# Kernel optimization log

Hardware: AMD Instinct MI355X
Metric: run time of the kernel (lower is better)

The kernel has to match this reference:

```python
import jax, jax.numpy as jnp
import numpy as np

# static sizes
B, N_PER, D, H, L, DFF, IN_DIM = 32, 1024, 128, 4, 3, 2048, 64
N = B * N_PER
HD = D // H
EPS = 1e-5


def setup_inputs() -> dict:
    key = jax.random.key(0)
    ks = jax.random.split(key, 16)
    s = 0.02
    rn = lambda k, shp: jax.random.normal(k, shp, jnp.float32) * s
    return {
        "x": jax.random.normal(ks[0], (N, IN_DIM), jnp.float32),
        # uniform graph sizes -> static max_nodes; sorted graph ids
        "batch": jnp.repeat(jnp.arange(B, dtype=jnp.int32), N_PER),
        "W_in": rn(ks[1], (D, IN_DIM)),
        "b_in": rn(ks[2], (D,)),
        "Wqkv": rn(ks[3], (L, 3 * D, D)),
        "bqkv": rn(ks[4], (L, 3 * D)),
        "Wo": rn(ks[5], (L, D, D)),
        "bo": rn(ks[6], (L, D)),
        "W1": rn(ks[7], (L, DFF, D)),
        "b1": rn(ks[8], (L, DFF)),
        "W2": rn(ks[9], (L, D, DFF)),
        "b2": rn(ks[10], (L, D)),
        "ln1_g": jnp.ones((L, D), jnp.float32),
        "ln1_b": jnp.zeros((L, D), jnp.float32),
        "ln2_g": jnp.ones((L, D), jnp.float32),
        "ln2_b": jnp.zeros((L, D), jnp.float32),
    }


def _ln(x, g, b):
    m = x.mean(-1, keepdims=True)
    v = jnp.mean((x - m) ** 2, axis=-1, keepdims=True)
    return (x - m) / jnp.sqrt(v + EPS) * g + b


def _mha(h, Wqkv, bqkv, Wo, bo):
    # h: [B, S, D]
    qkv = h @ Wqkv.T + bqkv                      # [B, S, 3D]
    q, k, v = jnp.split(qkv, 3, axis=-1)
    q = q.reshape(B, -1, H, HD)
    k = k.reshape(B, -1, H, HD)
    v = v.reshape(B, -1, H, HD)
    att = jnp.einsum("bqhd,bkhd->bhqk", q, k) / np.sqrt(HD).astype(np.float32)
    p = jax.nn.softmax(att, axis=-1)
    o = jnp.einsum("bhqk,bkhd->bqhd", p, v).reshape(B, -1, D)
    return o @ Wo.T + bo


def reference(x, batch, W_in, b_in, Wqkv, bqkv, Wo, bo, W1, b1, W2, b2,
              ln1_g, ln1_b, ln2_g, ln2_b):
    # fused ragged -> padded: project all nodes once, scatter by (graph, pos)
    h = x @ W_in.T + b_in                        # [N, D]
    starts = jnp.searchsorted(batch, jnp.arange(B, dtype=batch.dtype))
    pos = jnp.arange(N, dtype=batch.dtype) - starts[batch]
    padded = jnp.zeros((B, N_PER, D), h.dtype).at[batch, pos].set(h)

    out = padded
    for l in range(L):  # post-LN TransformerEncoderLayer, dropout=eval
        a = _mha(out, Wqkv[l], bqkv[l], Wo[l], bo[l])
        out = _ln(out + a, ln1_g[l], ln1_b[l])
        f = jax.nn.relu(out @ W1[l].T + b1[l]) @ W2[l].T + b2[l]
        out = _ln(out + f, ln2_g[l], ln2_b[l])

    # mask derived from projected inputs, exactly as the original
    mask = (padded.sum(axis=2) != 0).astype(out.dtype)  # [B, S]
    return (out * mask[:, :, None]).sum(axis=1) / mask.sum(axis=1, keepdims=True)
```

## Files before the change

### kernel.cpp

```cpp
#include <hip/hip_runtime.h>
#include <hip/hip_bf16.h>
#include <stdint.h>

#define BB    32
#define NPER  1024
#define NTOT  32768
#define DD    128
#define HH    4
#define HD    32
#define LL    3
#define DFF   2048
#define INDIM 64
#define QKSCALE 0.17677669529663687f

typedef unsigned short u16;
typedef short bf16x8 __attribute__((ext_vector_type(8)));
typedef float f32x4 __attribute__((ext_vector_type(4)));

#define AS_GLOBAL(p) ((const __attribute__((address_space(1))) void*)(p))
#define AS_LDS(p)    ((__attribute__((address_space(3))) void*)(p))

__device__ __forceinline__ float bf2f(u16 v){
  unsigned u = ((unsigned)v) << 16; float f; __builtin_memcpy(&f, &u, 4); return f;
}
__device__ __forceinline__ u16 f2bf(float f){
  unsigned u; __builtin_memcpy(&u, &f, 4);
  unsigned lsb = (u >> 16) & 1u;
  u += 0x7fffu + lsb;
  return (u16)(u >> 16);
}

constexpr size_t OFF_FLAG   = 0;
constexpr size_t OFF_STARTS = 256;
constexpr size_t OFF_BIN    = 1024;
constexpr size_t OFF_BQKV   = OFF_BIN   + 128*4;
constexpr size_t OFF_BO     = OFF_BQKV  + 1152*4;
constexpr size_t OFF_B1     = OFF_BO    + 384*4;
constexpr size_t OFF_B2     = OFF_B1    + 6144*4;
constexpr size_t OFF_LN1G   = OFF_B2    + 384*4;
constexpr size_t OFF_LN1B   = OFF_LN1G  + 384*4;
constexpr size_t OFF_LN2G   = OFF_LN1B  + 384*4;
constexpr size_t OFF_LN2B   = OFF_LN2G  + 384*4;
constexpr size_t OFF_XB     = 40960;
constexpr size_t OFF_WINB   = OFF_XB    + (size_t)2097152*2;
constexpr size_t OFF_WQKVB  = OFF_WINB  + (size_t)8192*2;
constexpr size_t OFF_WOB    = OFF_WQKVB + (size_t)147456*2;
constexpr size_t OFF_W1B    = OFF_WOB   + (size_t)49152*2;
constexpr size_t OFF_W2B    = OFF_W1B   + (size_t)786432*2;
constexpr size_t OFF_CUR    = OFF_W2B   + (size_t)786432*2;
constexpr size_t OFF_TMP    = OFF_CUR   + (size_t)4194304*4;
constexpr size_t OFF_CURB   = OFF_TMP   + (size_t)4194304*4;
constexpr size_t OFF_QKVB   = OFF_CURB  + (size_t)4194304*2;
constexpr size_t OFF_ATTNOB = OFF_QKVB  + (size_t)12582912*2;
constexpr size_t OFF_ACTB   = OFF_ATTNOB+ (size_t)4194304*2;
constexpr size_t OFF_MASK   = OFF_ACTB  + (size_t)16777216*2;
constexpr size_t OFF_VT     = OFF_MASK  + (size_t)NTOT*4;
constexpr size_t OFF_RED    = OFF_VT    + (size_t)4096*1024*2;
constexpr size_t OFF_CNT    = OFF_RED   + (size_t)32*8*128*4;

__device__ __forceinline__ int plaus(unsigned bits){
  if ((bits << 1) == 0u) return 1;
  unsigned e = (bits >> 23) & 0xFFu;
  return (e >= 100u && e <= 140u) ? 1 : 0;
}
__global__ void prep_kernel(const unsigned* __restrict__ x, const int* __restrict__ batch,
                            int* __restrict__ flag, int* __restrict__ starts){
  __shared__ int red[256];
  int t = threadIdx.x, c = 0;
  for (int i = t; i < 2048; i += 256){
    unsigned w = x[i];
    c += (plaus(w << 16) & plaus(w & 0xFFFF0000u));
  }
  red[t] = c; __syncthreads();
  for (int s = 128; s > 0; s >>= 1){ if (t < s) red[t] += red[t+s]; __syncthreads(); }
  if (t == 0) *flag = (red[0] >= 1229) ? 1 : 0;
  if (t < BB){
    int lo = 0, hi = NTOT;
    while (lo < hi){ int mid = (lo + hi) >> 1; if (batch[mid] < t) lo = mid + 1; else hi = mid; }
    starts[t] = lo;
  }
}

struct ConvSeg { const void* src; void* dst; int n; int tobf; };
struct ConvArgs { ConvSeg s[14]; };

__global__ __launch_bounds__(256) void convall_kernel(ConvArgs a, const int* __restrict__ flag){
  const int isb = *flag;
  const int blk = blockIdx.x;
  int seg = -1, base = 0, lb = 0;
  #pragma unroll
  for (int i = 0; i < 14; ++i){
    int nb = (a.s[i].n + 1023) >> 10;
    if (seg < 0){
      if (blk < base + nb){ seg = i; lb = blk - base; }
      base += nb;
    }
  }
  const ConvSeg sg = a.s[seg];
  const int idx = lb*1024 + threadIdx.x*4;
  if (idx >= sg.n) return;
  if (sg.tobf){
    u16* dst = (u16*)sg.dst + idx;
    if (isb){
      *(uint2*)dst = *(const uint2*)((const u16*)sg.src + idx);
    } else {
      const float* s4 = (const float*)sg.src + idx;
      dst[0] = f2bf(s4[0]); dst[1] = f2bf(s4[1]);
      dst[2] = f2bf(s4[2]); dst[3] = f2bf(s4[3]);
    }
  } else {
    float* dst = (float*)sg.dst + idx;
    if (isb){
      const u16* s4 = (const u16*)sg.src + idx;
      dst[0] = bf2f(s4[0]); dst[1] = bf2f(s4[1]);
      dst[2] = bf2f(s4[2]); dst[3] = bf2f(s4[3]);
    } else {
      *(float4*)dst = *(const float4*)((const float*)sg.src + idx);
    }
  }
}

__global__ __launch_bounds__(256) void inproj_kernel(
    const void* __restrict__ xraw,
    const u16* __restrict__ WINB,
    const float* __restrict__ bin,
    const int* __restrict__ batch, const int* __restrict__ starts,
    const int* __restrict__ flag,
    float* __restrict__ cur, u16* __restrict__ curb, float* __restrict__ mask)
{
  __shared__ __align__(16) u16 Wl[8192];
  const int t = threadIdx.x, wave = t >> 6, lane = t & 63;
  const int quad = lane >> 4, l16 = lane & 15;
  const int m0 = blockIdx.x * 64;
  const int isb = *flag;

  #pragma unroll
  for (int j = 0; j < 4; ++j){
    int s = t + 256*j;
    int r = s >> 3, c8 = (s & 7) ^ (r & 7);
    *(uint4*)&Wl[s*8] = *(const uint4*)(WINB + (size_t)r*INDIM + c8*8);
  }
  bf16x8 af[2];
  const int arow = m0 + wave*16 + l16;
  if (isb){
    const u16* XB = (const u16*)xraw;
    #pragma unroll
    for (int kk = 0; kk < 2; ++kk)
      af[kk] = *(const bf16x8*)(XB + (size_t)arow*INDIM + kk*32 + quad*8);
  } else {
    const float* Xf = (const float*)xraw;
    #pragma unroll
    for (int kk = 0; kk < 2; ++kk){
      float4 a = *(const float4*)(Xf + (size_t)arow*INDIM + kk*32 + quad*8);
      float4 b = *(const float4*)(Xf + (size_t)arow*INDIM + kk*32 + quad*8 + 4);
      af[kk][0] = (short)f2bf(a.x); af[kk][1] = (short)f2bf(a.y);
      af[kk][2] = (short)f2bf(a.z); af[kk][3] = (short)f2bf(a.w);
      af[kk][4] = (short)f2bf(b.x); af[kk][5] = (short)f2bf(b.y);
      af[kk][6] = (short)f2bf(b.z); af[kk][7] = (short)f2bf(b.w);
    }
  }
  __syncthreads();

  f32x4 O[8];
  #pragma unroll
  for (int nt = 0; nt < 8; ++nt){ O[nt][0]=0.f; O[nt][1]=0.f; O[nt][2]=0.f; O[nt][3]=0.f; }

  #pragma unroll
  for (int nt = 0; nt < 8; ++nt){
    int row = nt*16 + l16;
    bf16x8 wf[2];
    #pragma unroll
    for (int kk = 0; kk < 2; ++kk)
      wf[kk] = *(const bf16x8*)&Wl[(row*8 + ((kk*4 + quad) ^ (row & 7)))*8];
    #pragma unroll
    for (int kk = 0; kk < 2; ++kk)
      O[nt] = __builtin_amdgcn_mfma_f32_16x16x32_bf16(af[kk], wf[kk], O[nt], 0, 0, 0);
  }

  #pragma unroll
  for (int rr = 0; rr < 4; ++rr){
    int node = m0 + wave*16 + quad*4 + rr;
    int gr = batch[node];
    int p  = node - starts[gr];
    float vs[8], sum = 0.f;
    #pragma unroll
    for (int nt = 0; nt < 8; ++nt){
      float v = O[nt][rr] + bin[nt*16 + l16];
      vs[nt] = v; sum += v;
    }
    sum += __shfl_xor(sum, 1); sum += __shfl_xor(sum, 2);
    sum += __shfl_xor(sum, 4); sum += __shfl_xor(sum, 8);
    if ((unsigned)p < (unsigned)NPER && (unsigned)gr < (unsigned)BB){
      size_t j = (size_t)gr*NPER + p;
      #pragma unroll
      for (int nt = 0; nt < 8; ++nt){
        int col = nt*16 + l16;
        cur[j*DD + col]  = vs[nt];
        curb[j*DD + col] = f2bf(vs[nt]);
      }
      if (l16 == 0) mask[j] = (sum != 0.f) ? 1.f : 0.f;
    }
  }
}

__global__ __launch_bounds__(256) void fattn_kernel(
    const u16* __restrict__ qkvb,
    const u16* __restrict__ vt,
    u16* __restrict__ attnob)
{
  __shared__ __align__(16) u16 Klds[2][2048];
  __shared__ __align__(16) u16 Vl[2][2048];
  __shared__ __align__(16) u16 Pl[4][2][16*72];

  const int t = threadIdx.x;
  const int wave = t >> 6, lane = t & 63;
  const int quad = lane >> 4, l16 = lane & 15;
  const int q0 = blockIdx.x * 128;
  const int h = blockIdx.y, b = blockIdx.z;
  const size_t qkvbase = (size_t)b * NPER * 384;
  const u16* Kg = qkvb + qkvbase + 128 + h*HD;
  const u16* Vg = vt + (size_t)((b*HH + h)*HD) * NPER;

  bf16x8 qf[2];
  #pragma unroll
  for (int qt = 0; qt < 2; ++qt){
    const u16* qp = qkvb + qkvbase + (size_t)(q0 + wave*32 + qt*16 + l16)*384 + h*HD + quad*8;
    uint4 qv = *(const uint4*)qp;
    u16 raw[8]; __builtin_memcpy(raw, &qv, 16);
    #pragma unroll
    for (int j = 0; j < 8; ++j) qf[qt][j] = (short)f2bf(bf2f(raw[j]) * QKSCALE);
  }

  const int vcv = wave*2 + (lane >> 5), vd = lane & 31;
  auto stage = [&](int buf, int kt){
    __builtin_amdgcn_global_load_lds(
        AS_GLOBAL(Kg + (size_t)(kt*64 + lane)*384 + wave*8),
        AS_LDS(&Klds[buf][wave*64*8]), 16, 0, 0);
    __builtin_amdgcn_global_load_lds(
        AS_GLOBAL(Vg + (size_t)vd*NPER + kt*64 + vcv*8),
        AS_LDS(&Vl[buf][wave*64*8]), 16, 0, 0);
  };

  float lsum[2] = {0.f, 0.f};
  f32x4 o[2][2];
  #pragma unroll
  for (int qt = 0; qt < 2; ++qt)
    #pragma unroll
    for (int i = 0; i < 2; ++i){ o[qt][i][0]=0.f; o[qt][i][1]=0.f; o[qt][i][2]=0.f; o[qt][i][3]=0.f; }

  stage(0, 0);
  asm volatile("s_waitcnt vmcnt(0)" ::: "memory");
  __syncthreads();

  for (int kt = 0; kt < 16; ++kt){
    const int buf = kt & 1;
    if (kt + 1 < 16) stage(buf ^ 1, kt + 1);

    f32x4 sfr[2][4];
    #pragma unroll
    for (int nt = 0; nt < 4; ++nt){
      bf16x8 kf = *(const bf16x8*)&Klds[buf][(quad*64 + nt*16 + l16)*8];
      f32x4 z = {0.f,0.f,0.f,0.f};
      sfr[0][nt] = __builtin_amdgcn_mfma_f32_16x16x32_bf16(kf, qf[0], z, 0, 0, 0);
      sfr[1][nt] = __builtin_amdgcn_mfma_f32_16x16x32_bf16(kf, qf[1], z, 0, 0, 0);
    }

    #pragma unroll
    for (int qt = 0; qt < 2; ++qt){
      float ps = 0.f;
      #pragma unroll
      for (int nt = 0; nt < 4; ++nt){
        float e0 = __expf(sfr[qt][nt][0]), e1 = __expf(sfr[qt][nt][1]);
        float e2 = __expf(sfr[qt][nt][2]), e3 = __expf(sfr[qt][nt][3]);
        ps += (e0 + e1) + (e2 + e3);
        uint2 w;
        w.x = (unsigned)f2bf(e0) | ((unsigned)f2bf(e1) << 16);
        w.y = (unsigned)f2bf(e2) | ((unsigned)f2bf(e3) << 16);
        *(uint2*)&Pl[wave][qt][l16*72 + nt*16 + quad*4] = w;
      }
      ps += __shfl_xor(ps, 16);
      ps += __shfl_xor(ps, 32);
      lsum[qt] += ps;
    }
    asm volatile("s_waitcnt lgkmcnt(0)" ::: "memory");

    #pragma unroll
    for (int kk = 0; kk < 2; ++kk){
      bf16x8 v0 = *(const bf16x8*)&Vl[buf][((kk*4 + quad)*32 + l16)*8];
      bf16x8 v1 = *(const bf16x8*)&Vl[buf][((kk*4 + quad)*32 + 16 + l16)*8];
      #pragma unroll
      for (int qt = 0; qt < 2; ++qt){
        bf16x8 pf = *(const bf16x8*)&Pl[wave][qt][l16*72 + kk*32 + quad*8];
        o[qt][0] = __builtin_amdgcn_mfma_f32_16x16x32_bf16(pf, v0, o[qt][0], 0, 0, 0);
        o[qt][1] = __builtin_amdgcn_mfma_f32_16x16x32_bf16(pf, v1, o[qt][1], 0, 0, 0);
      }
    }

    if (kt + 1 < 16){
      asm volatile("s_waitcnt vmcnt(0)" ::: "memory");
      __syncthreads();
    }
  }

  #pragma unroll
  for (int qt = 0; qt < 2; ++qt){
    #pragma unroll
    for (int r = 0; r < 4; ++r){
      float inv = 1.f / __shfl(lsum[qt], quad*4 + r);
      int row = q0 + wave*32 + qt*16 + quad*4 + r;
      size_t base = (size_t)(b*NPER + row)*DD + h*HD;
      attnob[base + l16]      = f2bf(o[qt][0][r] * inv);
      attnob[base + 16 + l16] = f2bf(o[qt][1][r] * inv);
    }
  }
}

__global__ __launch_bounds__(256) void wgemm2_kernel(
    const u16* __restrict__ A,
    const u16* __restrict__ Wbase,
    const float* __restrict__ biasb,
    u16* __restrict__ outb, int opitch,
    u16* __restrict__ vtout)
{
  __shared__ __align__(16) u16 Wl[16384];
  const int t = threadIdx.x, wave = t >> 6, lane = t & 63;
  const int quad = lane >> 4, l16 = lane & 15;
  const int m0 = blockIdx.x * 128, nb = blockIdx.y;
  const u16* Wsl = Wbase + (size_t)nb * 16384;
  const float* bias = biasb + nb * 128;

  #pragma unroll
  for (int j = 0; j < 8; ++j){
    int s = t + 256*j;
    int r = s >> 4, cx = (s & 15) ^ (r & 15);
    *(uint4*)&Wl[s*8] = *(const uint4*)(Wsl + (size_t)r*128 + cx*8);
  }
  bf16x8 af[2][4];
  #pragma unroll
  for (int mt = 0; mt < 2; ++mt)
    #pragma unroll
    for (int kk = 0; kk < 4; ++kk)
      af[mt][kk] = *(const bf16x8*)(A + (size_t)(m0 + wave*32 + mt*16 + l16)*128 + kk*32 + quad*8);
  __syncthreads();

  f32x4 O[2][8];
  #pragma unroll
  for (int mt = 0; mt < 2; ++mt)
    #pragma unroll
    for (int nt = 0; nt < 8; ++nt){ O[mt][nt][0]=0.f; O[mt][nt][1]=0.f; O[mt][nt][2]=0.f; O[mt][nt][3]=0.f; }

  #pragma unroll
  for (int nt = 0; nt < 8; ++nt){
    int row = nt*16 + l16;
    bf16x8 wf[4];
    #pragma unroll
    for (int kk = 0; kk < 4; ++kk)
      wf[kk] = *(const bf16x8*)&Wl[(row*16 + ((kk*4 + quad) ^ l16))*8];
    #pragma unroll
    for (int mt = 0; mt < 2; ++mt)
      #pragma unroll
      for (int kk = 0; kk < 4; ++kk)
        O[mt][nt] = __builtin_amdgcn_mfma_f32_16x16x32_bf16(af[mt][kk], wf[kk], O[mt][nt], 0, 0, 0);
  }

  if (nb == 2){
    #pragma unroll
    for (int mt = 0; mt < 2; ++mt){
      int rowb = m0 + wave*32 + mt*16 + quad*4;
      int bg = rowb >> 10, s = rowb & 1023;
      #pragma unroll
      for (int nt = 0; nt < 8; ++nt){
        int col = nt*16 + l16;
        int hh = col >> 5, d = col & 31;
        float v0 = O[mt][nt][0] + bias[col], v1 = O[mt][nt][1] + bias[col];
        float v2 = O[mt][nt][2] + bias[col], v3 = O[mt][nt][3] + bias[col];
        uint2 w;
        w.x = (unsigned)f2bf(v0) | ((unsigned)f2bf(v1) << 16);
        w.y = (unsigned)f2bf(v2) | ((unsigned)f2bf(v3) << 16);
        *(uint2*)(vtout + (size_t)((bg*HH + hh)*HD + d)*NPER + s) = w;
      }
    }
  } else {
    #pragma unroll
    for (int mt = 0; mt < 2; ++mt)
      #pragma unroll
      for (int rr = 0; rr < 4; ++rr){
        int row = m0 + wave*32 + mt*16 + quad*4 + rr;
        #pragma unroll
        for (int nt = 0; nt < 8; ++nt){
          int col = nt*16 + l16;
          outb[(size_t)row*opitch + nb*128 + col] = f2bf(O[mt][nt][rr] + bias[col]);
        }
      }
  }
}

__global__ __launch_bounds__(256, 2) void ffn_kernel(
    const u16* __restrict__ attnob,
    const u16* __restrict__ Wog,
    const float* __restrict__ bo,
    const float* __restrict__ g1, const float* __restrict__ beta1,
    const u16* __restrict__ W1g,
    const u16* __restrict__ W2g,
    const float* __restrict__ b1,
    const float* __restrict__ b2,
    const float* __restrict__ g2, const float* __restrict__ beta2,
    float* __restrict__ cur, u16* __restrict__ curb)
{
  __shared__ __align__(16) u16 SM[37376];
  const int t = threadIdx.x, wave = t >> 6, lane = t & 63;
  const int quad = lane >> 4, l16 = lane & 15;
  const int m0 = blockIdx.x * 64;
  u16* Pw = &SM[32768 + wave*1152];

  #pragma unroll
  for (int i = 0; i < 8; ++i){
    int s0 = wave*512 + i*64;
    int s = s0 + lane;
    int r = s >> 4, cx = (s & 15) ^ (r & 15);
    __builtin_amdgcn_global_load_lds(
        AS_GLOBAL(Wog + (size_t)r*128 + cx*8),
        AS_LDS(&SM[16384 + s0*8]), 16, 0, 0);
  }
  bf16x8 afo[4];
  #pragma unroll
  for (int kk = 0; kk < 4; ++kk)
    afo[kk] = *(const bf16x8*)(attnob + (size_t)(m0 + wave*16 + l16)*128 + kk*32 + quad*8);
  asm volatile("s_waitcnt vmcnt(0)" ::: "memory");
  __syncthreads();

  f32x4 O[8];
  #pragma unroll
  for (int nt = 0; nt < 8; ++nt){ O[nt][0]=0.f; O[nt][1]=0.f; O[nt][2]=0.f; O[nt][3]=0.f; }
  #pragma unroll
  for (int nt = 0; nt < 8; ++nt){
    int row = nt*16 + l16;
    bf16x8 wf[4];
    #pragma unroll
    for (int kk = 0; kk < 4; ++kk)
      wf[kk] = *(const bf16x8*)&SM[16384 + (row*16 + ((kk*4 + quad) ^ l16))*8];
    #pragma unroll
    for (int kk = 0; kk < 4; ++kk)
      O[nt] = __builtin_amdgcn_mfma_f32_16x16x32_bf16(afo[kk], wf[kk], O[nt], 0, 0, 0);
  }

  float res[8][4];
  u16* Tw = &SM[wave*2176];
  #pragma unroll
  for (int rr = 0; rr < 4; ++rr){
    int row = m0 + wave*16 + quad*4 + rr;
    float vs[8], sum = 0.f;
    #pragma unroll
    for (int nt = 0; nt < 8; ++nt){
      int col = nt*16 + l16;
      float v = O[nt][rr] + bo[col] + cur[(size_t)row*DD + col];
      vs[nt] = v; sum += v;
    }
    sum += __shfl_xor(sum, 1); sum += __shfl_xor(sum, 2);
    sum += __shfl_xor(sum, 4); sum += __shfl_xor(sum, 8);
    float mean = sum * (1.f/DD);
    float sq = 0.f;
    #pragma unroll
    for (int nt = 0; nt < 8; ++nt){ float d = vs[nt] - mean; sq += d*d; }
    sq += __shfl_xor(sq, 1); sq += __shfl_xor(sq, 2);
    sq += __shfl_xor(sq, 4); sq += __shfl_xor(sq, 8);
    float rs = rsqrtf(sq * (1.f/DD) + 1e-5f);
    #pragma unroll
    for (int nt = 0; nt < 8; ++nt){
      int col = nt*16 + l16;
      float o = (vs[nt] - mean)*rs*g1[col] + beta1[col];
      res[nt][rr] = o;
      Tw[(quad*4 + rr)*136 + col] = f2bf(o);
    }
  }
  asm volatile("s_waitcnt lgkmcnt(0)" ::: "memory");

  bf16x8 af[4];
  #pragma unroll
  for (int kk = 0; kk < 4; ++kk)
    af[kk] = *(const bf16x8*)&Tw[l16*136 + kk*32 + quad*8];
  __syncthreads();

  auto stage = [&](int buf, int dffc){
    #pragma unroll
    for (int i = 0; i < 4; ++i){
      const int s0 = wave*256 + i*64;
      const int s  = s0 + lane;
      { int r = s >> 4, cx = (s & 15) ^ (r & 15);
        __builtin_amdgcn_global_load_lds(
            AS_GLOBAL(W1g + (size_t)(dffc + r)*128 + cx*8),
            AS_LDS(&SM[buf*8192 + s0*8]), 16, 0, 0); }
      { int r = s >> 3, cx = (s & 7) ^ (r & 7);
        __builtin_amdgcn_global_load_lds(
            AS_GLOBAL(W2g + (size_t)r*DFF + dffc + cx*8),
            AS_LDS(&SM[16384 + buf*8192 + s0*8]), 16, 0, 0); }
    }
  };

  #pragma unroll
  for (int nt = 0; nt < 8; ++nt){ O[nt][0]=0.f; O[nt][1]=0.f; O[nt][2]=0.f; O[nt][3]=0.f; }

  stage(0, 0);
  asm volatile("s_waitcnt vmcnt(0)" ::: "memory");
  __syncthreads();

  for (int c = 0; c < 32; ++c){
    const int buf = c & 1;
    if (c + 1 < 32) stage(buf ^ 1, (c + 1)*64);

    #pragma unroll
    for (int nt = 0; nt < 4; ++nt){
      int row = nt*16 + l16;
      bf16x8 wf[4];
      #pragma unroll
      for (int kk = 0; kk < 4; ++kk)
        wf[kk] = *(const bf16x8*)&SM[buf*8192 + (row*16 + ((kk*4 + quad) ^ l16))*8];
      float b1v = b1[c*64 + row];
      f32x4 s = {0.f,0.f,0.f,0.f};
      #pragma unroll
      for (int kk = 0; kk < 4; ++kk)
        s = __builtin_amdgcn_mfma_f32_16x16x32_bf16(af[kk], wf[kk], s, 0, 0, 0);
      #pragma unroll
      for (int rr = 0; rr < 4; ++rr)
        Pw[(quad*4 + rr)*72 + nt*16 + l16] = f2bf(fmaxf(s[rr] + b1v, 0.f));
    }
    asm volatile("s_waitcnt lgkmcnt(0)" ::: "memory");

    bf16x8 pf[2];
    #pragma unroll
    for (int kk = 0; kk < 2; ++kk)
      pf[kk] = *(const bf16x8*)&Pw[l16*72 + kk*32 + quad*8];
    #pragma unroll
    for (int nt = 0; nt < 8; ++nt){
      int row = nt*16 + l16;
      bf16x8 wf[2];
      #pragma unroll
      for (int kk = 0; kk < 2; ++kk)
        wf[kk] = *(const bf16x8*)&SM[16384 + buf*8192 + (row*8 + ((kk*4 + quad) ^ (l16 & 7)))*8];
      #pragma unroll
      for (int kk = 0; kk < 2; ++kk)
        O[nt] = __builtin_amdgcn_mfma_f32_16x16x32_bf16(pf[kk], wf[kk], O[nt], 0, 0, 0);
    }

    if (c + 1 < 32){
      asm volatile("s_waitcnt vmcnt(0)" ::: "memory");
      __syncthreads();
    }
  }

  #pragma unroll
  for (int rr = 0; rr < 4; ++rr){
    int row = m0 + wave*16 + quad*4 + rr;
    float vs[8], sum = 0.f;
    #pragma unroll
    for (int nt = 0; nt < 8; ++nt){
      int col = nt*16 + l16;
      float v = O[nt][rr] + b2[col] + res[nt][rr];
      vs[nt] = v; sum += v;
    }
    sum += __shfl_xor(sum, 1); sum += __shfl_xor(sum, 2);
    sum += __shfl_xor(sum, 4); sum += __shfl_xor(sum, 8);
    float mean = sum * (1.f/DD);
    float sq = 0.f;
    #pragma unroll
    for (int nt = 0; nt < 8; ++nt){ float d = vs[nt] - mean; sq += d*d; }
    sq += __shfl_xor(sq, 1); sq += __shfl_xor(sq, 2);
    sq += __shfl_xor(sq, 4); sq += __shfl_xor(sq, 8);
    float rs = rsqrtf(sq * (1.f/DD) + 1e-5f);
    #pragma unroll
    for (int nt = 0; nt < 8; ++nt){
      int col = nt*16 + l16;
      float o = (vs[nt] - mean)*rs*g2[col] + beta2[col];
      cur[(size_t)row*DD + col]  = o;
      curb[(size_t)row*DD + col] = f2bf(o);
    }
  }
}

__global__ __launch_bounds__(128) void reduce1_kernel(
    const float* __restrict__ cur, const float* __restrict__ mask,
    float* __restrict__ partial, float* __restrict__ cnt)
{
  int b = blockIdx.x, c = blockIdx.y, t = threadIdx.x;
  float acc = 0.f, cn = 0.f;
  for (int s = c*128; s < c*128 + 128; ++s){
    float mk = mask[b*NPER + s];
    acc += cur[(size_t)(b*NPER + s)*DD + t] * mk;
    cn += mk;
  }
  partial[(size_t)(b*8 + c)*DD + t] = acc;
  if (t == 0) cnt[b*8 + c] = cn;
}
__global__ __launch_bounds__(128) void reduce2_kernel(
    const float* __restrict__ partial, const float* __restrict__ cnt,
    const int* __restrict__ flag, void* __restrict__ out)
{
  int b = blockIdx.x, t = threadIdx.x;
  float acc = 0.f, cn = 0.f;
  #pragma unroll
  for (int c = 0; c < 8; ++c){
    acc += partial[(size_t)(b*8 + c)*DD + t];
    cn  += cnt[b*8 + c];
  }
  float val = acc / cn;
  if (*flag) ((u16*)out)[b*DD + t] = f2bf(val);
  else       ((float*)out)[b*DD + t] = val;
}

extern "C" void kernel_launch(void* const* d_in, const int* in_sizes, int n_in,
                              void* d_out, int out_size, void* d_ws, size_t ws_size,
                              hipStream_t stream)
{
  (void)in_sizes; (void)n_in; (void)out_size; (void)ws_size;
  char* ws = (char*)d_ws;
  int*   flag   = (int*)(ws + OFF_FLAG);
  int*   starts = (int*)(ws + OFF_STARTS);
  float* BIN  = (float*)(ws + OFF_BIN);
  float* BQKV = (float*)(ws + OFF_BQKV);
  float* BO   = (float*)(ws + OFF_BO);
  float* B1   = (float*)(ws + OFF_B1);
  float* B2   = (float*)(ws + OFF_B2);
  float* LN1G = (float*)(ws + OFF_LN1G);
  float* LN1B = (float*)(ws + OFF_LN1B);
  float* LN2G = (float*)(ws + OFF_LN2G);
  float* LN2B = (float*)(ws + OFF_LN2B);
  u16* WINB  = (u16*)(ws + OFF_WINB);
  u16* WQKVB = (u16*)(ws + OFF_WQKVB);
  u16* WOB   = (u16*)(ws + OFF_WOB);
  u16* W1B   = (u16*)(ws + OFF_W1B);
  u16* W2B   = (u16*)(ws + OFF_W2B);
  float* CUR = (float*)(ws + OFF_CUR);
  u16* CURB  = (u16*)(ws + OFF_CURB);
  u16* QKVB  = (u16*)(ws + OFF_QKVB);
  u16* ATTNOB= (u16*)(ws + OFF_ATTNOB);
  float* MASK= (float*)(ws + OFF_MASK);
  u16* VT    = (u16*)(ws + OFF_VT);
  float* RED = (float*)(ws + OFF_RED);
  float* CNT = (float*)(ws + OFF_CNT);

  prep_kernel<<<1, 256, 0, stream>>>((const unsigned*)d_in[0], (const int*)d_in[1],
                                     flag, starts);

  ConvArgs ca;
  ca.s[0]  = { d_in[2],  WINB,  DD*INDIM,   1 };
  ca.s[1]  = { d_in[4],  WQKVB, LL*3*DD*DD, 1 };
  ca.s[2]  = { d_in[6],  WOB,   LL*DD*DD,   1 };
  ca.s[3]  = { d_in[8],  W1B,   LL*DFF*DD,  1 };
  ca.s[4]  = { d_in[10], W2B,   LL*DD*DFF,  1 };
  ca.s[5]  = { d_in[3],  BIN,   DD,         0 };
  ca.s[6]  = { d_in[5],  BQKV,  LL*3*DD,    0 };
  ca.s[7]  = { d_in[7],  BO,    LL*DD,      0 };
  ca.s[8]  = { d_in[9],  B1,    LL*DFF,     0 };
  ca.s[9]  = { d_in[11], B2,    LL*DD,      0 };
  ca.s[10] = { d_in[12], LN1G,  LL*DD,      0 };
  ca.s[11] = { d_in[13], LN1B,  LL*DD,      0 };
  ca.s[12] = { d_in[14], LN2G,  LL*DD,      0 };
  ca.s[13] = { d_in[15], LN2B,  LL*DD,      0 };
  int nblk = 0;
  for (int i = 0; i < 14; ++i) nblk += (ca.s[i].n + 1023) >> 10;
  convall_kernel<<<nblk, 256, 0, stream>>>(ca, flag);

  inproj_kernel<<<NTOT/64, 256, 0, stream>>>(
      d_in[0], WINB, BIN, (const int*)d_in[1], starts, flag, CUR, CURB, MASK);

  for (int l = 0; l < LL; ++l){
    wgemm2_kernel<<<dim3(NTOT/128, 3), 256, 0, stream>>>(
        CURB, WQKVB + (size_t)l*3*DD*DD, BQKV + l*3*DD, QKVB, 384, VT);
    fattn_kernel<<<dim3(NPER/128, HH, BB), 256, 0, stream>>>(QKVB, VT, ATTNOB);
    ffn_kernel<<<dim3(NTOT/64), 256, 0, stream>>>(
        ATTNOB, WOB + (size_t)l*DD*DD, BO + l*DD, LN1G + l*DD, LN1B + l*DD,
        W1B + (size_t)l*DFF*DD, W2B + (size_t)l*DD*DFF,
        B1 + l*DFF, B2 + l*DD, LN2G + l*DD, LN2B + l*DD, CUR, CURB);
  }

  reduce1_kernel<<<dim3(BB, 8), 128, 0, stream>>>(CUR, MASK, RED, CNT);
  reduce2_kernel<<<BB, 128, 0, stream>>>(RED, CNT, flag, d_out);
}
```

Before: 479.5 us.

## Store Q/K/V in per-head, tile-packed layouts so attention loads are contiguous

The QKV projection now writes Q as per-(graph,head) row-major blocks, and K and V^T in pre-tiled layouts that match the LDS staging order of the attention kernel. Attention staging then reads contiguous 16-byte chunks instead of strided 384-element rows, which is meant to improve global-to-LDS coalescing. The cost moves to scattered, finer-grained stores in the projection epilogue. The K buffer is carved from the old QKV workspace at an offset, which assumes that region is large enough.

After: 477.1 us. About the same (-0.5%).

```diff
diff --git a/kernel.cpp b/kernel.cpp
--- a/kernel.cpp
+++ b/kernel.cpp
@@ -204,8 +204,9 @@
 }
 
 __global__ __launch_bounds__(256) void fattn_kernel(
-    const u16* __restrict__ qkvb,
-    const u16* __restrict__ vt,
+    const u16* __restrict__ qh,
+    const u16* __restrict__ ktb,
+    const u16* __restrict__ vtb,
     u16* __restrict__ attnob)
 {
   __shared__ __align__(16) u16 Klds[2][2048];
@@ -217,27 +218,26 @@
   const int quad = lane >> 4, l16 = lane & 15;
   const int q0 = blockIdx.x * 128;
   const int h = blockIdx.y, b = blockIdx.z;
-  const size_t qkvbase = (size_t)b * NPER * 384;
-  const u16* Kg = qkvb + qkvbase + 128 + h*HD;
-  const u16* Vg = vt + (size_t)((b*HH + h)*HD) * NPER;
+  const size_t bh = (size_t)(b*HH + h) * NPER * 32;
+  const u16* Qg = qh + bh;
+  const u16* Kg = ktb + bh;
+  const u16* Vg = vtb + bh;
 
   bf16x8 qf[2];
   #pragma unroll
   for (int qt = 0; qt < 2; ++qt){
-    const u16* qp = qkvb + qkvbase + (size_t)(q0 + wave*32 + qt*16 + l16)*384 + h*HD + quad*8;
-    uint4 qv = *(const uint4*)qp;
+    uint4 qv = *(const uint4*)(Qg + (size_t)(q0 + wave*32 + qt*16 + l16)*32 + quad*8);
     u16 raw[8]; __builtin_memcpy(raw, &qv, 16);
     #pragma unroll
     for (int j = 0; j < 8; ++j) qf[qt][j] = (short)f2bf(bf2f(raw[j]) * QKSCALE);
   }
 
-  const int vcv = wave*2 + (lane >> 5), vd = lane & 31;
   auto stage = [&](int buf, int kt){
     __builtin_amdgcn_global_load_lds(
-        AS_GLOBAL(Kg + (size_t)(kt*64 + lane)*384 + wave*8),
+        AS_GLOBAL(Kg + kt*2048 + wave*512 + lane*8),
         AS_LDS(&Klds[buf][wave*64*8]), 16, 0, 0);
     __builtin_amdgcn_global_load_lds(
-        AS_GLOBAL(Vg + (size_t)vd*NPER + kt*64 + vcv*8),
+        AS_GLOBAL(Vg + kt*2048 + wave*512 + lane*8),
         AS_LDS(&Vl[buf][wave*64*8]), 16, 0, 0);
   };
 
@@ -319,8 +319,7 @@
     const u16* __restrict__ A,
     const u16* __restrict__ Wbase,
     const float* __restrict__ biasb,
-    u16* __restrict__ outb, int opitch,
-    u16* __restrict__ vtout)
+    u16* __restrict__ qh, u16* __restrict__ ktb, u16* __restrict__ vtb)
 {
   __shared__ __align__(16) u16 Wl[16384];
   const int t = threadIdx.x, wave = t >> 6, lane = t & 63;
@@ -363,35 +362,51 @@
         O[mt][nt] = __builtin_amdgcn_mfma_f32_16x16x32_bf16(af[mt][kk], wf[kk], O[mt][nt], 0, 0, 0);
   }
 
-  if (nb == 2){
+  if (nb == 0){
+    #pragma unroll
+    for (int mt = 0; mt < 2; ++mt)
+      #pragma unroll
+      for (int rr = 0; rr < 4; ++rr){
+        int s = m0 + wave*32 + mt*16 + quad*4 + rr;
+        int bg = s >> 10, sl = s & 1023;
+        #pragma unroll
+        for (int nt = 0; nt < 8; ++nt){
+          int col = nt*16 + l16, hh = col >> 5, d = col & 31;
+          qh[((size_t)(bg*HH + hh)*NPER + sl)*32 + d] = f2bf(O[mt][nt][rr] + bias[col]);
+        }
+      }
+  } else if (nb == 1){
+    #pragma unroll
+    for (int mt = 0; mt < 2; ++mt)
+      #pragma unroll
+      for (int rr = 0; rr < 4; ++rr){
+        int s = m0 + wave*32 + mt*16 + quad*4 + rr;
+        int bg = s >> 10, sl = s & 1023;
+        int kt = sl >> 6, r = sl & 63;
+        #pragma unroll
+        for (int nt = 0; nt < 8; ++nt){
+          int col = nt*16 + l16, hh = col >> 5, d = col & 31;
+          ktb[(size_t)(bg*HH + hh)*NPER*32 + kt*2048 + (d>>3)*512 + r*8 + (d&7)]
+              = f2bf(O[mt][nt][rr] + bias[col]);
+        }
+      }
+  } else {
     #pragma unroll
     for (int mt = 0; mt < 2; ++mt){
       int rowb = m0 + wave*32 + mt*16 + quad*4;
-      int bg = rowb >> 10, s = rowb & 1023;
+      int bg = rowb >> 10, sl = rowb & 1023;
+      int kt = sl >> 6, cv = (sl & 63) >> 3, j0 = sl & 7;
       #pragma unroll
       for (int nt = 0; nt < 8; ++nt){
-        int col = nt*16 + l16;
-        int hh = col >> 5, d = col & 31;
+        int col = nt*16 + l16, hh = col >> 5, d = col & 31;
         float v0 = O[mt][nt][0] + bias[col], v1 = O[mt][nt][1] + bias[col];
         float v2 = O[mt][nt][2] + bias[col], v3 = O[mt][nt][3] + bias[col];
         uint2 w;
         w.x = (unsigned)f2bf(v0) | ((unsigned)f2bf(v1) << 16);
         w.y = (unsigned)f2bf(v2) | ((unsigned)f2bf(v3) << 16);
-        *(uint2*)(vtout + (size_t)((bg*HH + hh)*HD + d)*NPER + s) = w;
+        *(uint2*)(vtb + (size_t)(bg*HH + hh)*NPER*32 + kt*2048 + cv*256 + d*8 + j0) = w;
       }
     }
-  } else {
-    #pragma unroll
-    for (int mt = 0; mt < 2; ++mt)
-      #pragma unroll
-      for (int rr = 0; rr < 4; ++rr){
-        int row = m0 + wave*32 + mt*16 + quad*4 + rr;
-        #pragma unroll
-        for (int nt = 0; nt < 8; ++nt){
-          int col = nt*16 + l16;
-          outb[(size_t)row*opitch + nb*128 + col] = f2bf(O[mt][nt][rr] + bias[col]);
-        }
-      }
   }
 }
 
@@ -631,10 +646,11 @@
   u16* W2B   = (u16*)(ws + OFF_W2B);
   float* CUR = (float*)(ws + OFF_CUR);
   u16* CURB  = (u16*)(ws + OFF_CURB);
-  u16* QKVB  = (u16*)(ws + OFF_QKVB);
+  u16* QH    = (u16*)(ws + OFF_QKVB);
+  u16* KT    = (u16*)(ws + OFF_QKVB + (size_t)4194304*2);
   u16* ATTNOB= (u16*)(ws + OFF_ATTNOB);
   float* MASK= (float*)(ws + OFF_MASK);
-  u16* VT    = (u16*)(ws + OFF_VT);
+  u16* VTB   = (u16*)(ws + OFF_VT);
   float* RED = (float*)(ws + OFF_RED);
   float* CNT = (float*)(ws + OFF_CNT);
 
@@ -665,8 +681,8 @@
 
   for (int l = 0; l < LL; ++l){
     wgemm2_kernel<<<dim3(NTOT/128, 3), 256, 0, stream>>>(
-        CURB, WQKVB + (size_t)l*3*DD*DD, BQKV + l*3*DD, QKVB, 384, VT);
-    fattn_kernel<<<dim3(NPER/128, HH, BB), 256, 0, stream>>>(QKVB, VT, ATTNOB);
+        CURB, WQKVB + (size_t)l*3*DD*DD, BQKV + l*3*DD, QH, KT, VTB);
+    fattn_kernel<<<dim3(NPER/128, HH, BB), 256, 0, stream>>>(QH, KT, VTB, ATTNOB);
     ffn_kernel<<<dim3(NTOT/64), 256, 0, stream>>>(
         ATTNOB, WOB + (size_t)l*DD*DD, BO + l*DD, LN1G + l*DD, LN1B + l*DD,
         W1B + (size_t)l*DFF*DD, W2B + (size_t)l*DD*DFF,
```
